# Kernel optimization log

Measured on AMD Instinct MI355X. Metric: run time of the kernel, lower is better.

Reference implementation:

```python
import jax, jax.numpy as jnp
import numpy as np

N_NODES = 20000


def _segment_softmax(alpha, dst, num_nodes):
    # numerically-stable softmax over edges grouped by destination node
    m = jax.ops.segment_max(alpha, dst, num_segments=num_nodes)
    m = jnp.where(jnp.isfinite(m), m, 0.0)
    a = jnp.exp(alpha - m[dst])
    denom = jax.ops.segment_sum(a, dst, num_segments=num_nodes)
    return a / denom[dst]


def mgcn_conv(x, src, dst, edge_type, basis, att, weight, root, bias, num_nodes):
    # x: [N, in], basis: [B, in, out], att: [R, B], weight: [R, out=in]
    x_i = x[dst]                                   # [E, in] target feats
    x_j = x[src]                                   # [E, in] source feats
    # per-edge attention logit: sum_d x_i[d] * w_r[d] * x_j[d]
    alpha = jnp.sum(x_i * weight[edge_type] * x_j, axis=1)   # [E]
    alpha = _segment_softmax(alpha, dst, num_nodes)          # [E]
    # basis-decomposed per-edge transform: x_j @ (att_r . basis)
    t = jnp.einsum('ei,bio->ebo', x_j, basis)                # [E, B, out]
    msg = jnp.einsum('ebo,eb->eo', t, att[edge_type])        # [E, out]
    msg = msg * alpha[:, None]
    out = jax.ops.segment_sum(msg, dst, num_segments=num_nodes)  # [N, out]
    return out + x @ root + bias


def setup_inputs() -> dict:
    key = jax.random.key(0)
    ks = jax.random.split(key, 16)
    E, D, R, B, N = 32768, 128, 474, 64, N_NODES
    s = 0.05
    return {
        'entity': jnp.arange(N, dtype=jnp.int64) if jax.config.jax_enable_x64 else jnp.arange(N, dtype=jnp.int32),
        'edge_index': jax.random.randint(ks[0], (2, E), 0, N, dtype=jnp.int32),
        'edge_type': jax.random.randint(ks[1], (E,), 0, R, dtype=jnp.int32),
        'emb_table': jax.random.normal(ks[2], (N, D), dtype=jnp.float32),
        'basis1': jax.random.normal(ks[3], (B, D, D), dtype=jnp.float32) * s,
        'att1': jax.random.normal(ks[4], (R, B), dtype=jnp.float32) * s,
        'weight1': jax.random.normal(ks[5], (R, D), dtype=jnp.float32) * s,
        'root1': jax.random.normal(ks[6], (D, D), dtype=jnp.float32) * s,
        'bias1': jnp.zeros((D,), dtype=jnp.float32),
        'basis2': jax.random.normal(ks[7], (B, D, D), dtype=jnp.float32) * s,
        'att2': jax.random.normal(ks[8], (R, B), dtype=jnp.float32) * s,
        'weight2': jax.random.normal(ks[9], (R, D), dtype=jnp.float32) * s,
        'root2': jax.random.normal(ks[10], (D, D), dtype=jnp.float32) * s,
        'bias2': jnp.zeros((D,), dtype=jnp.float32),
    }


def reference(entity, edge_index, edge_type, emb_table,
              basis1, att1, weight1, root1, bias1,
              basis2, att2, weight2, root2, bias2):
    src, dst = edge_index[0], edge_index[1]   # PyG: (source j, target i)
    x = emb_table[entity]                     # embedding lookup
    h = jax.nn.relu(mgcn_conv(x, src, dst, edge_type, basis1, att1,
                              weight1, root1, bias1, N_NODES))
    # dropout is identity at inference
    out = mgcn_conv(h, src, dst, edge_type, basis2, att2,
                    weight2, root2, bias2, N_NODES)
    return out
```

## Files before the change

### kernel.cpp

```cpp
#include <hip/hip_runtime.h>
#include <hip/hip_bf16.h>

#define N_NODES 20000
#define N_EDGES 32768
#define DIM 128
#define N_REL 474
#define N_BASIS 64
#define TILE_E 64
#define CHCAP 128
#define MAXCH (N_EDGES / CHCAP + N_REL)
#define WSTRIDE 264
#define HIST_BLKS 16
#define EDGES_PER_HIST (N_EDGES / HIST_BLKS)

#define WMIX_BLKS 1024
#define ROOTT_BLKS 2
#define GATHER_BASE (WMIX_BLKS + ROOTT_BLKS)
#define PREP_GRID 1664

#define RG_BLKS ((N_NODES + 63) / 64)
#define MSG_GRID (MAXCH + RG_BLKS)
#define MERGE_GRID 1024

typedef __bf16 bf16x8 __attribute__((ext_vector_type(8)));
typedef float f32x4 __attribute__((ext_vector_type(4)));

__device__ __forceinline__ unsigned short f2b(float f) {
    unsigned u = __float_as_uint(f);
    unsigned r = (u + 0x7FFFu + ((u >> 16) & 1u)) >> 16;
    return (unsigned short)r;
}
__device__ __forceinline__ float b2f(unsigned short s) {
    return __uint_as_float(((unsigned)s) << 16);
}
__device__ __forceinline__ __bf16 u2b(unsigned short u) {
    union { unsigned short u; __bf16 b; } c; c.u = u; return c.b;
}
__device__ __forceinline__ float dot2bf(unsigned a, unsigned b, float wx, float wy) {
    return b2f((unsigned short)(a & 0xFFFFu)) * wx * b2f((unsigned short)(b & 0xFFFFu))
         + b2f((unsigned short)(a >> 16)) * wy * b2f((unsigned short)(b >> 16));
}

__global__ __launch_bounds__(256) void prep_kernel(const float4* __restrict__ emb,
                                                   const int* __restrict__ entity,
                                                   const int* __restrict__ etype,
                                                   ushort4* __restrict__ xb4,
                                                   float4* __restrict__ zreg, int zcount4,
                                                   int* __restrict__ partial,
                                                   const float* __restrict__ att1,
                                                   const float* __restrict__ basis1,
                                                   unsigned short* __restrict__ W1,
                                                   const float* __restrict__ att2,
                                                   const float* __restrict__ basis2,
                                                   unsigned short* __restrict__ W2,
                                                   const float* __restrict__ root1,
                                                   unsigned short* __restrict__ rootT1,
                                                   const float* __restrict__ root2,
                                                   unsigned short* __restrict__ rootT2) {
    __shared__ __align__(16) unsigned short bt[64 * WSTRIDE];
    int t = threadIdx.x;
    if (blockIdx.x < WMIX_BLKS) {
        int wi = blockIdx.x;
        int layer = wi >> 9;
        int cb = (wi >> 3) & 63;
        int rg = wi & 7;
        const float* att   = layer ? att2 : att1;
        const float* basis = layer ? basis2 : basis1;
        unsigned short* W  = layer ? W2 : W1;
        int io0 = cb * 256;
        int r0 = rg * 64;
#pragma unroll
        for (int p = 0; p < 16; p++) {
            int c = t + 256 * p;
            int k = c >> 6, of = c & 63;
            float4 v = *(const float4*)(basis + (size_t)k * (DIM * DIM) + io0 + of * 4);
            ushort4 s;
            s.x = f2b(v.x); s.y = f2b(v.y); s.z = f2b(v.z); s.w = f2b(v.w);
            int ofx = of ^ (((k >> 3) & 7) << 2);
            *(ushort4*)&bt[k * WSTRIDE + ofx * 4] = s;
        }
        __syncthreads();

        int w = t >> 6, l = t & 63, n = l & 15, q = l >> 4;
        bf16x8 bfr[2][4];
#pragma unroll
        for (int kb = 0; kb < 2; kb++) {
            int kbase = kb * 32 + q * 8;
            int sx = ((kb * 4 + q) & 7) << 4;
#pragma unroll
            for (int c = 0; c < 4; c++) {
                int ob = (w * 64 + c * 16 + n) ^ sx;
#pragma unroll
                for (int j = 0; j < 8; j++) bfr[kb][c][j] = u2b(bt[(kbase + j) * WSTRIDE + ob]);
            }
        }
        __syncthreads();

        f32x4 acc[4][4] = {};
#pragma unroll
        for (int kb = 0; kb < 2; kb++) {
            int kbase = kb * 32 + q * 8;
            bf16x8 a[4];
#pragma unroll
            for (int rt = 0; rt < 4; rt++) {
                int rm = min(r0 + rt * 16 + n, N_REL - 1);
                const float4* ap = (const float4*)(att + (size_t)rm * N_BASIS + kbase);
                float4 u0 = ap[0], u1 = ap[1];
                a[rt][0] = (__bf16)u0.x; a[rt][1] = (__bf16)u0.y;
                a[rt][2] = (__bf16)u0.z; a[rt][3] = (__bf16)u0.w;
                a[rt][4] = (__bf16)u1.x; a[rt][5] = (__bf16)u1.y;
                a[rt][6] = (__bf16)u1.z; a[rt][7] = (__bf16)u1.w;
            }
#pragma unroll
            for (int c = 0; c < 4; c++) {
#pragma unroll
                for (int rt = 0; rt < 4; rt++)
                    acc[rt][c] = __builtin_amdgcn_mfma_f32_16x16x32_bf16(a[rt], bfr[kb][c], acc[rt][c], 0, 0, 0);
            }
        }
#pragma unroll
        for (int rt = 0; rt < 4; rt++) {
#pragma unroll
            for (int c = 0; c < 4; c++) {
#pragma unroll
                for (int g = 0; g < 4; g++)
                    bt[(rt * 16 + q * 4 + g) * WSTRIDE + w * 64 + c * 16 + n] = f2b(acc[rt][c][g]);
            }
        }
        __syncthreads();
        int srow = t >> 2, sseg = t & 3;
        int rr = r0 + srow;
        if (rr < N_REL) {
            const int4* sp = (const int4*)&bt[srow * WSTRIDE];
            unsigned short* wp = W + (size_t)rr * (DIM * DIM) + io0;
#pragma unroll
            for (int ii = 0; ii < 8; ii++) {
                int i = (ii + sseg * 2) & 7;
                int4 v = sp[sseg * 8 + i];
                *(int4*)(wp + sseg * 64 + i * 8) = v;
            }
        }
    } else if (blockIdx.x < GATHER_BASE) {
        int wi2 = blockIdx.x - WMIX_BLKS;
        const float* rm = wi2 ? root2 : root1;
        unsigned short* rt_ = wi2 ? rootT2 : rootT1;
        unsigned short* sb16 = bt;
#pragma unroll
        for (int p = 0; p < 16; p++) {
            int idx = t + 256 * p;
            int k = idx >> 5, o4 = idx & 31;
            float4 v = ((const float4*)rm)[idx];
            ushort4 s;
            s.x = f2b(v.x); s.y = f2b(v.y); s.z = f2b(v.z); s.w = f2b(v.w);
            *(ushort4*)&sb16[k * 132 + o4 * 4] = s;
        }
        __syncthreads();
        int o = t >> 1, kh = (t & 1) * 64;
#pragma unroll
        for (int i = 0; i < 16; i++) {
            int k0 = kh + i * 4;
            ushort4 s;
            s.x = sb16[(k0 + 0) * 132 + o];
            s.y = sb16[(k0 + 1) * 132 + o];
            s.z = sb16[(k0 + 2) * 132 + o];
            s.w = sb16[(k0 + 3) * 132 + o];
            *(ushort4*)&rt_[o * DIM + k0] = s;
        }
    } else {
        int pb = blockIdx.x - GATHER_BASE;
        int gtid = pb * 256 + t;
        int gsz = (PREP_GRID - GATHER_BASE) * 256;
        int total4 = N_NODES * DIM / 4;
        for (int i = gtid; i < total4; i += gsz) {
            int n = i >> 5, rem = i & 31;
            float4 v = emb[(size_t)entity[n] * 32 + rem];
            ushort4 s;
            s.x = f2b(v.x); s.y = f2b(v.y); s.z = f2b(v.z); s.w = f2b(v.w);
            xb4[i] = s;
        }
        float4 z = make_float4(0.f, 0.f, 0.f, 0.f);
        for (int i = gtid; i < zcount4; i += gsz) zreg[i] = z;
        if (pb < HIST_BLKS) {
            int* ih = (int*)bt;
            for (int i = t; i < N_REL; i += 256) ih[i] = 0;
            __syncthreads();
            int e0 = pb * EDGES_PER_HIST;
            for (int e = e0 + t; e < e0 + EDGES_PER_HIST; e += 256)
                atomicAdd(&ih[etype[e]], 1);
            __syncthreads();
            for (int i = t; i < N_REL; i += 256) partial[pb * N_REL + i] = ih[i];
        }
    }
}

__global__ void scanr_kernel(const int* __restrict__ partial, int* __restrict__ offs,
                             int* __restrict__ cursor, int* __restrict__ chunk_r,
                             int* __restrict__ chunk_o, int* __restrict__ nchunks) {
    __shared__ int s[512];
    __shared__ int lnc;
    int t = threadIdx.x;
    int v = 0;
    if (t < N_REL) {
#pragma unroll
        for (int k = 0; k < HIST_BLKS; k++) v += partial[k * N_REL + t];
    }
    s[t] = v;
    if (t == 0) lnc = 0;
    __syncthreads();
    for (int d = 1; d < 512; d <<= 1) {
        int add = (t >= d) ? s[t - d] : 0;
        __syncthreads();
        s[t] += add;
        __syncthreads();
    }
    int excl = s[t] - v;
    if (t < N_REL) { offs[t] = excl; cursor[t] = excl; }
    if (t == 0) offs[N_REL] = N_EDGES;
    if (t < N_REL && v > 0) {
        int nc = (v + CHCAP - 1) / CHCAP;
        int cb = atomicAdd(&lnc, nc);
        for (int c = 0; c < nc; c++) { chunk_r[cb + c] = t; chunk_o[cb + c] = excl + c * CHCAP; }
    }
    __syncthreads();
    if (t == 0) *nchunks = lnc;
}

__global__ __launch_bounds__(256) void scatter_kernel(const int* __restrict__ etype,
                                                      int* __restrict__ cursor,
                                                      int* __restrict__ eids) {
    for (int e = blockIdx.x * 256 + threadIdx.x; e < N_EDGES; e += (int)gridDim.x * 256) {
        int r = etype[e];
        int p = atomicAdd(&cursor[r], 1);
        eids[p] = e;
    }
}

__global__ __launch_bounds__(256) void msg_kernel(const unsigned short* __restrict__ xb,
                                                  const unsigned short* __restrict__ W,
                                                  const float* __restrict__ wlog,
                                                  const int* __restrict__ src,
                                                  const int* __restrict__ dst,
                                                  const int* __restrict__ eids,
                                                  const int* __restrict__ offs,
                                                  const int* __restrict__ chunk_r,
                                                  const int* __restrict__ chunk_o,
                                                  const int* __restrict__ nchunks,
                                                  float* __restrict__ den,
                                                  float* __restrict__ accm,
                                                  const unsigned short* __restrict__ rootT,
                                                  float* __restrict__ racc) {
    __shared__ __align__(16) unsigned short wt[128 * 136];
    __shared__ __align__(16) float wf[DIM];
    __shared__ float scf[TILE_E];
    __shared__ int sdd[TILE_E];
    __shared__ int ssrc[TILE_E];

    int t = threadIdx.x;
    if ((int)blockIdx.x < MAXCH) {
        if ((int)blockIdx.x >= *nchunks) return;
        int r = chunk_r[blockIdx.x];
        int base = chunk_o[blockIdx.x];
        int cnt = min(base + CHCAP, offs[r + 1]) - base;
        const unsigned short* Wr = W + (size_t)r * (DIM * DIM);
#pragma unroll
        for (int p = 0; p < 8; p++) {
            int c = t + 256 * p;
            int k = c >> 4, oct = c & 15;
            int4 v = *(const int4*)(Wr + k * DIM + oct * 8);
            int oct2 = oct ^ (((k >> 3) & 7) << 1);
            *(int4*)&wt[k * 136 + oct2 * 8] = v;
        }
        if (t < 32) ((float4*)wf)[t] = ((const float4*)(wlog + (size_t)r * DIM))[t];
        __syncthreads();

        int w = t >> 6, l = t & 63, n = l & 15, q = l >> 4;
        int el4 = t >> 2, l4 = t & 3;

        for (int t0 = 0; t0 < cnt; t0 += TILE_E) {
            int nE = min(TILE_E, cnt - t0);
            if (t < TILE_E) {
                if (t < nE) {
                    int e = eids[base + t0 + t];
                    ssrc[t] = src[e];
                    sdd[t]  = dst[e];
                } else { ssrc[t] = 0; sdd[t] = 0; }
            }
            __syncthreads();

            {
                int s_ = ssrc[el4], d_ = sdd[el4];
                const int4* xj = (const int4*)(xb + (size_t)s_ * DIM) + l4 * 4;
                const int4* xi = (const int4*)(xb + (size_t)d_ * DIM) + l4 * 4;
                const float4* wv = (const float4*)&wf[l4 * 32];
                float v = 0.f;
#pragma unroll
                for (int u = 0; u < 4; u++) {
                    int4 a = xj[u]; int4 bb = xi[u];
                    float4 w0 = wv[u * 2], w1 = wv[u * 2 + 1];
                    v += dot2bf((unsigned)a.x, (unsigned)bb.x, w0.x, w0.y)
                       + dot2bf((unsigned)a.y, (unsigned)bb.y, w0.z, w0.w)
                       + dot2bf((unsigned)a.z, (unsigned)bb.z, w1.x, w1.y)
                       + dot2bf((unsigned)a.w, (unsigned)bb.w, w1.z, w1.w);
                }
                v += __shfl_xor(v, 1, 64);
                v += __shfl_xor(v, 2, 64);
                if (l4 == 0) {
                    if (el4 < nE) {
                        float a = expf(v);
                        scf[el4] = a;
                        atomicAdd(&den[d_], a);
                    } else scf[el4] = 0.f;
                }
            }
            __syncthreads();

            f32x4 acc[2][4] = {};
#pragma unroll
            for (int kb = 0; kb < 4; kb++) {
                bf16x8 a[4];
#pragma unroll
                for (int rt = 0; rt < 4; rt++)
                    a[rt] = *(const bf16x8*)(xb + (size_t)ssrc[rt * 16 + n] * DIM + kb * 32 + q * 8);
                int kbase = kb * 32 + q * 8;
                int sx = ((kb * 4 + q) & 7) << 4;
#pragma unroll
                for (int c = 0; c < 2; c++) {
                    int ob = ((w * 2 + c) * 16 + n) ^ sx;
                    bf16x8 bb;
#pragma unroll
                    for (int j = 0; j < 8; j++) bb[j] = u2b(wt[(kbase + j) * 136 + ob]);
#pragma unroll
                    for (int rt = 0; rt < 4; rt++)
                        acc[c][rt] = __builtin_amdgcn_mfma_f32_16x16x32_bf16(a[rt], bb, acc[c][rt], 0, 0, 0);
                }
            }
#pragma unroll
            for (int c = 0; c < 2; c++) {
                int col = (w * 2 + c) * 16 + n;
#pragma unroll
                for (int rt = 0; rt < 4; rt++) {
#pragma unroll
                    for (int rg = 0; rg < 4; rg++) {
                        int e = rt * 16 + q * 4 + rg;
                        if (e < nE)
                            atomicAdd(&accm[(size_t)sdd[e] * DIM + col], scf[e] * acc[c][rt][rg]);
                    }
                }
            }
            __syncthreads();
        }
    } else {
        int n0 = ((int)blockIdx.x - MAXCH) * 64;
        unsigned short* xrf = wt;
#pragma unroll
        for (int p = 0; p < 4; p++) {
            int c = t + 256 * p;
            int g = c >> 6;
            int rt = g >> 2, kb = g & 3;
            int q2 = (c >> 4) & 3, m = c & 15;
            int row = n0 + rt * 16 + m;
            int oct = kb * 4 + q2;
            int4 v = make_int4(0, 0, 0, 0);
            if (row < N_NODES) v = *(const int4*)(xb + (size_t)row * DIM + oct * 8);
            *(int4*)&xrf[c * 8] = v;
        }
        __syncthreads();

        int w_ = t >> 6, l = t & 63, n = l & 15, q = l >> 4;
        f32x4 acc[2][4] = {};
#pragma unroll
        for (int kb = 0; kb < 4; kb++) {
            bf16x8 a[4];
#pragma unroll
            for (int rt = 0; rt < 4; rt++) a[rt] = *(const bf16x8*)&xrf[((rt * 4 + kb) * 64 + l) * 8];
            int kbase = kb * 32 + q * 8;
#pragma unroll
            for (int c = 0; c < 2; c++) {
                int col = (w_ * 2 + c) * 16 + n;
                bf16x8 bb = *(const bf16x8*)(rootT + (size_t)col * DIM + kbase);
#pragma unroll
                for (int rt = 0; rt < 4; rt++)
                    acc[c][rt] = __builtin_amdgcn_mfma_f32_16x16x32_bf16(a[rt], bb, acc[c][rt], 0, 0, 0);
            }
        }
#pragma unroll
        for (int c = 0; c < 2; c++) {
            int col = (w_ * 2 + c) * 16 + n;
#pragma unroll
            for (int rt = 0; rt < 4; rt++) {
#pragma unroll
                for (int rg = 0; rg < 4; rg++) {
                    int row = n0 + rt * 16 + q * 4 + rg;
                    if (row < N_NODES)
                        racc[(size_t)row * DIM + col] = acc[c][rt][rg];
                }
            }
        }
    }
}

__global__ __launch_bounds__(256) void merge_kernel(const float4* __restrict__ racc,
                                                    const float4* __restrict__ accm,
                                                    const float* __restrict__ den,
                                                    const float* __restrict__ bias,
                                                    float4* __restrict__ outf,
                                                    ushort4* __restrict__ outb) {
    int gtid = blockIdx.x * 256 + threadIdx.x;
    const int tot4 = N_NODES * (DIM / 4);
    for (int i = gtid; i < tot4; i += (int)gridDim.x * 256) {
        int row = i >> 5;
        int c0 = (i & 31) * 4;
        float4 rv = racc[i];
        float4 mv = accm[i];
        float4 bo = *(const float4*)&bias[c0];
        float dv = den[row];
        float inv = dv > 0.f ? 1.0f / dv : 0.f;
        float4 v;
        v.x = rv.x + bo.x + mv.x * inv;
        v.y = rv.y + bo.y + mv.y * inv;
        v.z = rv.z + bo.z + mv.z * inv;
        v.w = rv.w + bo.w + mv.w * inv;
        if (outb) {
            ushort4 s;
            s.x = f2b(fmaxf(v.x, 0.f)); s.y = f2b(fmaxf(v.y, 0.f));
            s.z = f2b(fmaxf(v.z, 0.f)); s.w = f2b(fmaxf(v.w, 0.f));
            outb[i] = s;
        } else {
            outf[i] = v;
        }
    }
}

extern "C" void kernel_launch(void* const* d_in, const int* in_sizes, int n_in,
                              void* d_out, int out_size, void* d_ws, size_t ws_size,
                              hipStream_t stream) {
    const int N = N_NODES, E = N_EDGES, R = N_REL;

    const int* entity = (const int*)d_in[0];
    const int* eidx   = (const int*)d_in[1];
    const int* src    = eidx;
    const int* dst    = eidx + E;
    const int* etype  = (const int*)d_in[2];
    const float* emb  = (const float*)d_in[3];
    const float* basis1 = (const float*)d_in[4];
    const float* att1   = (const float*)d_in[5];
    const float* w1     = (const float*)d_in[6];
    const float* root1  = (const float*)d_in[7];
    const float* bias1  = (const float*)d_in[8];
    const float* basis2 = (const float*)d_in[9];
    const float* att2   = (const float*)d_in[10];
    const float* w2     = (const float*)d_in[11];
    const float* root2  = (const float*)d_in[12];
    const float* bias2  = (const float*)d_in[13];
    float* out = (float*)d_out;

    size_t off = 0;
    auto alloc = [&](size_t bytes) -> void* {
        void* p = (char*)d_ws + off;
        off += (bytes + 255) & ~(size_t)255;
        return p;
    };
    unsigned short* W1 = (unsigned short*)alloc((size_t)R * DIM * DIM * 2);
    unsigned short* W2 = (unsigned short*)alloc((size_t)R * DIM * DIM * 2);
    unsigned short* xb = (unsigned short*)alloc((size_t)N * DIM * 2);
    unsigned short* hb = (unsigned short*)alloc((size_t)N * DIM * 2);
    float* racc1  = (float*)alloc((size_t)N * DIM * 4);
    float* racc2  = (float*)alloc((size_t)N * DIM * 4);
    float* zreg   = (float*)alloc(((size_t)2 * N + (size_t)2 * N * DIM) * 4);
    float* den1   = zreg;
    float* den2   = zreg + N;
    float* accm1  = zreg + 2 * N;
    float* accm2  = zreg + 2 * N + (size_t)N * DIM;
    unsigned short* rootT1 = (unsigned short*)alloc((size_t)DIM * DIM * 2);
    unsigned short* rootT2 = (unsigned short*)alloc((size_t)DIM * DIM * 2);
    int* partial  = (int*)alloc((size_t)HIST_BLKS * R * 4);
    int* offs     = (int*)alloc((size_t)(R + 1) * 4);
    int* cursor   = (int*)alloc((size_t)R * 4);
    int* eids     = (int*)alloc((size_t)E * 4);
    int* chunk_r  = (int*)alloc((size_t)MAXCH * 4);
    int* chunk_o  = (int*)alloc((size_t)MAXCH * 4);
    int* nchunks  = (int*)alloc(256);

    int zcount4 = (2 * N + 2 * N * DIM) / 4;

    prep_kernel<<<PREP_GRID, 256, 0, stream>>>(
        (const float4*)emb, entity, etype, (ushort4*)xb, (float4*)zreg, zcount4, partial,
        att1, basis1, W1, att2, basis2, W2, root1, rootT1, root2, rootT2);

    scanr_kernel<<<1, 512, 0, stream>>>(partial, offs, cursor, chunk_r, chunk_o, nchunks);
    scatter_kernel<<<64, 256, 0, stream>>>(etype, cursor, eids);

    msg_kernel<<<MSG_GRID, 256, 0, stream>>>(xb, W1, w1, src, dst, eids, offs,
                                             chunk_r, chunk_o, nchunks,
                                             den1, accm1, rootT1, racc1);
    merge_kernel<<<MERGE_GRID, 256, 0, stream>>>((const float4*)racc1, (const float4*)accm1,
                                                 den1, bias1, nullptr, (ushort4*)hb);

    msg_kernel<<<MSG_GRID, 256, 0, stream>>>(hb, W2, w2, src, dst, eids, offs,
                                             chunk_r, chunk_o, nchunks,
                                             den2, accm2, rootT2, racc2);
    merge_kernel<<<MERGE_GRID, 256, 0, stream>>>((const float4*)racc2, (const float4*)accm2,
                                                 den2, bias2, (float4*)out, nullptr);
}
```

Measured before the change: 212.0 us.

## Split prep into basis conversion and fused wmix/plan/root-GEMM kernel

```diff
diff --git a/kernel.cpp b/kernel.cpp
--- a/kernel.cpp
+++ b/kernel.cpp
@@ -9,17 +9,16 @@
 #define TILE_E 64
 #define CHCAP 128
 #define MAXCH (N_EDGES / CHCAP + N_REL)
-#define WSTRIDE 264
 #define HIST_BLKS 16
 #define EDGES_PER_HIST (N_EDGES / HIST_BLKS)
 
-#define WMIX_BLKS 1024
-#define ROOTT_BLKS 2
-#define GATHER_BASE (WMIX_BLKS + ROOTT_BLKS)
-#define PREP_GRID 1664
-
+#define PRE_GRID 1024
+#define BST 136
+#define WMIX2_BLKS 2048
 #define RG_BLKS ((N_NODES + 63) / 64)
-#define MSG_GRID (MAXCH + RG_BLKS)
+#define WP_GRID (WMIX2_BLKS + 1 + RG_BLKS)
+#define MSG1_GRID MAXCH
+#define MSG2_GRID (MAXCH + RG_BLKS)
 #define MERGE_GRID 1024
 
 typedef __bf16 bf16x8 __attribute__((ext_vector_type(8)));
@@ -41,62 +40,140 @@
          + b2f((unsigned short)(a >> 16)) * wy * b2f((unsigned short)(b >> 16));
 }
 
-__global__ __launch_bounds__(256) void prep_kernel(const float4* __restrict__ emb,
-                                                   const int* __restrict__ entity,
-                                                   const int* __restrict__ etype,
-                                                   ushort4* __restrict__ xb4,
-                                                   float4* __restrict__ zreg, int zcount4,
-                                                   int* __restrict__ partial,
-                                                   const float* __restrict__ att1,
-                                                   const float* __restrict__ basis1,
-                                                   unsigned short* __restrict__ W1,
-                                                   const float* __restrict__ att2,
-                                                   const float* __restrict__ basis2,
-                                                   unsigned short* __restrict__ W2,
-                                                   const float* __restrict__ root1,
-                                                   unsigned short* __restrict__ rootT1,
-                                                   const float* __restrict__ root2,
-                                                   unsigned short* __restrict__ rootT2) {
-    __shared__ __align__(16) unsigned short bt[64 * WSTRIDE];
+__global__ __launch_bounds__(256) void pre_kernel(const float4* __restrict__ emb,
+                                                  const int* __restrict__ entity,
+                                                  const int* __restrict__ etype,
+                                                  ushort4* __restrict__ xb4,
+                                                  float4* __restrict__ zreg, int zcount4,
+                                                  int* __restrict__ partial,
+                                                  const float* __restrict__ basis1,
+                                                  ushort4* __restrict__ bas16_1,
+                                                  const float* __restrict__ basis2,
+                                                  ushort4* __restrict__ bas16_2,
+                                                  const float* __restrict__ root1,
+                                                  unsigned short* __restrict__ rootT1,
+                                                  const float* __restrict__ root2,
+                                                  unsigned short* __restrict__ rootT2) {
+    __shared__ __align__(16) unsigned short sb16[128 * 132];
     int t = threadIdx.x;
-    if (blockIdx.x < WMIX_BLKS) {
-        int wi = blockIdx.x;
-        int layer = wi >> 9;
-        int cb = (wi >> 3) & 63;
-        int rg = wi & 7;
-        const float* att   = layer ? att2 : att1;
-        const float* basis = layer ? basis2 : basis1;
-        unsigned short* W  = layer ? W2 : W1;
-        int io0 = cb * 256;
-        int r0 = rg * 64;
+    if (blockIdx.x < 2) {
+        const float* rm = blockIdx.x ? root2 : root1;
+        unsigned short* rt_ = blockIdx.x ? rootT2 : rootT1;
 #pragma unroll
         for (int p = 0; p < 16; p++) {
-            int c = t + 256 * p;
-            int k = c >> 6, of = c & 63;
-            float4 v = *(const float4*)(basis + (size_t)k * (DIM * DIM) + io0 + of * 4);
+            int idx = t + 256 * p;
+            int k = idx >> 5, o4 = idx & 31;
+            float4 v = ((const float4*)rm)[idx];
             ushort4 s;
             s.x = f2b(v.x); s.y = f2b(v.y); s.z = f2b(v.z); s.w = f2b(v.w);
+            *(ushort4*)&sb16[k * 132 + o4 * 4] = s;
+        }
+        __syncthreads();
+        int o = t >> 1, kh = (t & 1) * 64;
+#pragma unroll
+        for (int i = 0; i < 16; i++) {
+            int k0 = kh + i * 4;
+            ushort4 s;
+            s.x = sb16[(k0 + 0) * 132 + o];
+            s.y = sb16[(k0 + 1) * 132 + o];
+            s.z = sb16[(k0 + 2) * 132 + o];
+            s.w = sb16[(k0 + 3) * 132 + o];
+            *(ushort4*)&rt_[o * DIM + k0] = s;
+        }
+    } else {
+        int pb = blockIdx.x - 2;
+        int gtid = pb * 256 + t;
+        int gsz = (PRE_GRID - 2) * 256;
+        int total4 = N_NODES * DIM / 4;
+        for (int i = gtid; i < total4; i += gsz) {
+            int n = i >> 5, rem = i & 31;
+            float4 v = emb[(size_t)entity[n] * 32 + rem];
+            ushort4 s;
+            s.x = f2b(v.x); s.y = f2b(v.y); s.z = f2b(v.z); s.w = f2b(v.w);
+            xb4[i] = s;
+        }
+        float4 z = make_float4(0.f, 0.f, 0.f, 0.f);
+        for (int i = gtid; i < zcount4; i += gsz) zreg[i] = z;
+        int totb4 = N_BASIS * DIM * DIM / 4;
+        for (int i = gtid; i < totb4; i += gsz) {
+            float4 v = ((const float4*)basis1)[i];
+            ushort4 s;
+            s.x = f2b(v.x); s.y = f2b(v.y); s.z = f2b(v.z); s.w = f2b(v.w);
+            bas16_1[i] = s;
+        }
+        for (int i = gtid; i < totb4; i += gsz) {
+            float4 v = ((const float4*)basis2)[i];
+            ushort4 s;
+            s.x = f2b(v.x); s.y = f2b(v.y); s.z = f2b(v.z); s.w = f2b(v.w);
+            bas16_2[i] = s;
+        }
+        if (pb < HIST_BLKS) {
+            int* ih = (int*)sb16;
+            for (int i = t; i < N_REL; i += 256) ih[i] = 0;
+            __syncthreads();
+            int e0 = pb * EDGES_PER_HIST;
+            for (int e = e0 + t; e < e0 + EDGES_PER_HIST; e += 256)
+                atomicAdd(&ih[etype[e]], 1);
+            __syncthreads();
+            for (int i = t; i < N_REL; i += 256) partial[pb * N_REL + i] = ih[i];
+        }
+    }
+}
+
+__global__ __launch_bounds__(256) void wmixplan_kernel(const unsigned short* __restrict__ bas16_1,
+                                                       const float* __restrict__ att1,
+                                                       unsigned short* __restrict__ W1,
+                                                       const unsigned short* __restrict__ bas16_2,
+                                                       const float* __restrict__ att2,
+                                                       unsigned short* __restrict__ W2,
+                                                       const int* __restrict__ partial,
+                                                       int* __restrict__ offs,
+                                                       int* __restrict__ chunk_r,
+                                                       int* __restrict__ chunk_o,
+                                                       int* __restrict__ nchunks,
+                                                       int* __restrict__ eids,
+                                                       const int* __restrict__ etype,
+                                                       const unsigned short* __restrict__ xb,
+                                                       const unsigned short* __restrict__ rootT1,
+                                                       float* __restrict__ racc1) {
+    __shared__ __align__(16) unsigned short bt[64 * BST];
+    int t = threadIdx.x;
+    if (blockIdx.x < WMIX2_BLKS) {
+        int wi = blockIdx.x;
+        int layer = wi >> 10;
+        int cb = (wi >> 3) & 127;
+        int rg = wi & 7;
+        const unsigned short* bas = layer ? bas16_2 : bas16_1;
+        const float* att   = layer ? att2 : att1;
+        unsigned short* W  = layer ? W2 : W1;
+        int io0 = cb * 128;
+        int r0 = rg * 64;
+#pragma unroll
+        for (int p = 0; p < 8; p++) {
+            int c = t + 256 * p;
+            int k = c >> 5, of = c & 31;
+            ushort4 s = *(const ushort4*)(bas + (size_t)k * (DIM * DIM) + io0 + of * 4);
             int ofx = of ^ (((k >> 3) & 7) << 2);
-            *(ushort4*)&bt[k * WSTRIDE + ofx * 4] = s;
+            *(ushort4*)&bt[k * BST + ofx * 4] = s;
         }
         __syncthreads();
 
         int w = t >> 6, l = t & 63, n = l & 15, q = l >> 4;
-        bf16x8 bfr[2][4];
+        bf16x8 bfr[2][2];
 #pragma unroll
         for (int kb = 0; kb < 2; kb++) {
             int kbase = kb * 32 + q * 8;
             int sx = ((kb * 4 + q) & 7) << 4;
 #pragma unroll
-            for (int c = 0; c < 4; c++) {
-                int ob = (w * 64 + c * 16 + n) ^ sx;
-#pragma unroll
-                for (int j = 0; j < 8; j++) bfr[kb][c][j] = u2b(bt[(kbase + j) * WSTRIDE + ob]);
-            }
-        }
-        __syncthreads();
-
-        f32x4 acc[4][4] = {};
+            for (int c = 0; c < 2; c++) {
+                int ob = (w * 32 + c * 16 + n) ^ sx;
+#pragma unroll
+                for (int j = 0; j < 8; j++) bfr[kb][c][j] = u2b(bt[(kbase + j) * BST + ob]);
+            }
+        }
+        __syncthreads();
+
+        f32x4 acc[4][2] = {};
 #pragma unroll
         for (int kb = 0; kb < 2; kb++) {
             int kbase = kb * 32 + q * 8;
@@ -112,7 +189,7 @@
                 a[rt][6] = (__bf16)u1.z; a[rt][7] = (__bf16)u1.w;
             }
 #pragma unroll
-            for (int c = 0; c < 4; c++) {
+            for (int c = 0; c < 2; c++) {
 #pragma unroll
                 for (int rt = 0; rt < 4; rt++)
                     acc[rt][c] = __builtin_amdgcn_mfma_f32_16x16x32_bf16(a[rt], bfr[kb][c], acc[rt][c], 0, 0, 0);
@@ -121,117 +198,118 @@
 #pragma unroll
         for (int rt = 0; rt < 4; rt++) {
 #pragma unroll
-            for (int c = 0; c < 4; c++) {
+            for (int c = 0; c < 2; c++) {
 #pragma unroll
                 for (int g = 0; g < 4; g++)
-                    bt[(rt * 16 + q * 4 + g) * WSTRIDE + w * 64 + c * 16 + n] = f2b(acc[rt][c][g]);
+                    bt[(rt * 16 + q * 4 + g) * BST + w * 32 + c * 16 + n] = f2b(acc[rt][c][g]);
             }
         }
         __syncthreads();
         int srow = t >> 2, sseg = t & 3;
         int rr = r0 + srow;
         if (rr < N_REL) {
-            const int4* sp = (const int4*)&bt[srow * WSTRIDE];
             unsigned short* wp = W + (size_t)rr * (DIM * DIM) + io0;
-#pragma unroll
-            for (int ii = 0; ii < 8; ii++) {
-                int i = (ii + sseg * 2) & 7;
-                int4 v = sp[sseg * 8 + i];
-                *(int4*)(wp + sseg * 64 + i * 8) = v;
-            }
-        }
-    } else if (blockIdx.x < GATHER_BASE) {
-        int wi2 = blockIdx.x - WMIX_BLKS;
-        const float* rm = wi2 ? root2 : root1;
-        unsigned short* rt_ = wi2 ? rootT2 : rootT1;
-        unsigned short* sb16 = bt;
-#pragma unroll
-        for (int p = 0; p < 16; p++) {
-            int idx = t + 256 * p;
-            int k = idx >> 5, o4 = idx & 31;
-            float4 v = ((const float4*)rm)[idx];
-            ushort4 s;
-            s.x = f2b(v.x); s.y = f2b(v.y); s.z = f2b(v.z); s.w = f2b(v.w);
-            *(ushort4*)&sb16[k * 132 + o4 * 4] = s;
-        }
-        __syncthreads();
-        int o = t >> 1, kh = (t & 1) * 64;
-#pragma unroll
-        for (int i = 0; i < 16; i++) {
-            int k0 = kh + i * 4;
-            ushort4 s;
-            s.x = sb16[(k0 + 0) * 132 + o];
-            s.y = sb16[(k0 + 1) * 132 + o];
-            s.z = sb16[(k0 + 2) * 132 + o];
-            s.w = sb16[(k0 + 3) * 132 + o];
-            *(ushort4*)&rt_[o * DIM + k0] = s;
+            const int4* sp = (const int4*)&bt[srow * BST];
+#pragma unroll
+            for (int ii = 0; ii < 4; ii++) {
+                int i = (ii + sseg) & 3;
+                *(int4*)(wp + sseg * 32 + i * 8) = sp[sseg * 4 + i];
+            }
+        }
+    } else if (blockIdx.x == WMIX2_BLKS) {
+        int* sA   = (int*)bt;
+        int* sB   = sA + 512;
+        int* lcur = sB + 512;
+        __shared__ int lnc;
+        int t2 = t + 256;
+        int v0 = 0, v1 = 0;
+        if (t < N_REL) {
+#pragma unroll
+            for (int k = 0; k < HIST_BLKS; k++) v0 += partial[k * N_REL + t];
+        }
+        if (t2 < N_REL) {
+#pragma unroll
+            for (int k = 0; k < HIST_BLKS; k++) v1 += partial[k * N_REL + t2];
+        }
+        sA[t] = v0; sA[t2] = v1;
+        if (t == 0) lnc = 0;
+        __syncthreads();
+        int* src_ = sA; int* dst_ = sB;
+        for (int d = 1; d < 512; d <<= 1) {
+            int a0 = src_[t]  + ((t  >= d) ? src_[t  - d] : 0);
+            int a1 = src_[t2] + ((t2 >= d) ? src_[t2 - d] : 0);
+            dst_[t] = a0; dst_[t2] = a1;
+            __syncthreads();
+            int* tmp = src_; src_ = dst_; dst_ = tmp;
+        }
+        int e0 = src_[t] - v0, e1 = src_[t2] - v1;
+        if (t < N_REL)  { offs[t] = e0;  lcur[t] = e0; }
+        if (t2 < N_REL) { offs[t2] = e1; lcur[t2] = e1; }
+        if (t == 0) offs[N_REL] = N_EDGES;
+        if (t < N_REL && v0 > 0) {
+            int nc = (v0 + CHCAP - 1) / CHCAP;
+            int cb = atomicAdd(&lnc, nc);
+            for (int c = 0; c < nc; c++) { chunk_r[cb + c] = t;  chunk_o[cb + c] = e0 + c * CHCAP; }
+        }
+        if (t2 < N_REL && v1 > 0) {
+            int nc = (v1 + CHCAP - 1) / CHCAP;
+            int cb = atomicAdd(&lnc, nc);
+            for (int c = 0; c < nc; c++) { chunk_r[cb + c] = t2; chunk_o[cb + c] = e1 + c * CHCAP; }
+        }
+        __syncthreads();
+        if (t == 0) *nchunks = lnc;
+        for (int e = t; e < N_EDGES; e += 256) {
+            int r = etype[e];
+            int p = atomicAdd(&lcur[r], 1);
+            eids[p] = e;
         }
     } else {
-        int pb = blockIdx.x - GATHER_BASE;
-        int gtid = pb * 256 + t;
-        int gsz = (PREP_GRID - GATHER_BASE) * 256;
-        int total4 = N_NODES * DIM / 4;
-        for (int i = gtid; i < total4; i += gsz) {
-            int n = i >> 5, rem = i & 31;
-            float4 v = emb[(size_t)entity[n] * 32 + rem];
-            ushort4 s;
-            s.x = f2b(v.x); s.y = f2b(v.y); s.z = f2b(v.z); s.w = f2b(v.w);
-            xb4[i] = s;
-        }
-        float4 z = make_float4(0.f, 0.f, 0.f, 0.f);
-        for (int i = gtid; i < zcount4; i += gsz) zreg[i] = z;
-        if (pb < HIST_BLKS) {
-            int* ih = (int*)bt;
-            for (int i = t; i < N_REL; i += 256) ih[i] = 0;
-            __syncthreads();
-            int e0 = pb * EDGES_PER_HIST;
-            for (int e = e0 + t; e < e0 + EDGES_PER_HIST; e += 256)
-                atomicAdd(&ih[etype[e]], 1);
-            __syncthreads();
-            for (int i = t; i < N_REL; i += 256) partial[pb * N_REL + i] = ih[i];
-        }
-    }
-}
-
-__global__ void scanr_kernel(const int* __restrict__ partial, int* __restrict__ offs,
-                             int* __restrict__ cursor, int* __restrict__ chunk_r,
-                             int* __restrict__ chunk_o, int* __restrict__ nchunks) {
-    __shared__ int s[512];
-    __shared__ int lnc;
-    int t = threadIdx.x;
-    int v = 0;
-    if (t < N_REL) {
-#pragma unroll
-        for (int k = 0; k < HIST_BLKS; k++) v += partial[k * N_REL + t];
-    }
-    s[t] = v;
-    if (t == 0) lnc = 0;
-    __syncthreads();
-    for (int d = 1; d < 512; d <<= 1) {
-        int add = (t >= d) ? s[t - d] : 0;
-        __syncthreads();
-        s[t] += add;
-        __syncthreads();
-    }
-    int excl = s[t] - v;
-    if (t < N_REL) { offs[t] = excl; cursor[t] = excl; }
-    if (t == 0) offs[N_REL] = N_EDGES;
-    if (t < N_REL && v > 0) {
-        int nc = (v + CHCAP - 1) / CHCAP;
-        int cb = atomicAdd(&lnc, nc);
-        for (int c = 0; c < nc; c++) { chunk_r[cb + c] = t; chunk_o[cb + c] = excl + c * CHCAP; }
-    }
-    __syncthreads();
-    if (t == 0) *nchunks = lnc;
-}
-
-__global__ __launch_bounds__(256) void scatter_kernel(const int* __restrict__ etype,
-                                                      int* __restrict__ cursor,
-                                                      int* __restrict__ eids) {
-    for (int e = blockIdx.x * 256 + threadIdx.x; e < N_EDGES; e += (int)gridDim.x * 256) {
-        int r = etype[e];
-        int p = atomicAdd(&cursor[r], 1);
-        eids[p] = e;
+        int n0 = ((int)blockIdx.x - WMIX2_BLKS - 1) * 64;
+        unsigned short* xrf = bt;
+#pragma unroll
+        for (int p = 0; p < 4; p++) {
+            int c = t + 256 * p;
+            int g = c >> 6;
+            int rt = g >> 2, kb = g & 3;
+            int q2 = (c >> 4) & 3, m = c & 15;
+            int row = n0 + rt * 16 + m;
+            int oct = kb * 4 + q2;
+            int4 v = make_int4(0, 0, 0, 0);
+            if (row < N_NODES) v = *(const int4*)(xb + (size_t)row * DIM + oct * 8);
+            *(int4*)&xrf[c * 8] = v;
+        }
+        __syncthreads();
+
+        int w_ = t >> 6, l = t & 63, n = l & 15, q = l >> 4;
+        f32x4 acc[2][4] = {};
+#pragma unroll
+        for (int kb = 0; kb < 4; kb++) {
+            bf16x8 a[4];
+#pragma unroll
+            for (int rt = 0; rt < 4; rt++) a[rt] = *(const bf16x8*)&xrf[((rt * 4 + kb) * 64 + l) * 8];
+            int kbase = kb * 32 + q * 8;
+#pragma unroll
+            for (int c = 0; c < 2; c++) {
+                int col = (w_ * 2 + c) * 16 + n;
+                bf16x8 bb = *(const bf16x8*)(rootT1 + (size_t)col * DIM + kbase);
+#pragma unroll
+                for (int rt = 0; rt < 4; rt++)
+                    acc[c][rt] = __builtin_amdgcn_mfma_f32_16x16x32_bf16(a[rt], bb, acc[c][rt], 0, 0, 0);
+            }
+        }
+#pragma unroll
+        for (int c = 0; c < 2; c++) {
+            int col = (w_ * 2 + c) * 16 + n;
+#pragma unroll
+            for (int rt = 0; rt < 4; rt++) {
+#pragma unroll
+                for (int rg = 0; rg < 4; rg++) {
+                    int row = n0 + rt * 16 + q * 4 + rg;
+                    if (row < N_NODES)
+                        racc1[(size_t)row * DIM + col] = acc[c][rt][rg];
+                }
+            }
+        }
     }
 }
 
@@ -473,9 +551,10 @@
     float* accm2  = zreg + 2 * N + (size_t)N * DIM;
     unsigned short* rootT1 = (unsigned short*)alloc((size_t)DIM * DIM * 2);
     unsigned short* rootT2 = (unsigned short*)alloc((size_t)DIM * DIM * 2);
+    unsigned short* bas16_1 = (unsigned short*)alloc((size_t)N_BASIS * DIM * DIM * 2);
+    unsigned short* bas16_2 = (unsigned short*)alloc((size_t)N_BASIS * DIM * DIM * 2);
     int* partial  = (int*)alloc((size_t)HIST_BLKS * R * 4);
     int* offs     = (int*)alloc((size_t)(R + 1) * 4);
-    int* cursor   = (int*)alloc((size_t)R * 4);
     int* eids     = (int*)alloc((size_t)E * 4);
     int* chunk_r  = (int*)alloc((size_t)MAXCH * 4);
     int* chunk_o  = (int*)alloc((size_t)MAXCH * 4);
@@ -483,22 +562,25 @@
 
     int zcount4 = (2 * N + 2 * N * DIM) / 4;
 
-    prep_kernel<<<PREP_GRID, 256, 0, stream>>>(
+    pre_kernel<<<PRE_GRID, 256, 0, stream>>>(
         (const float4*)emb, entity, etype, (ushort4*)xb, (float4*)zreg, zcount4, partial,
-        att1, basis1, W1, att2, basis2, W2, root1, rootT1, root2, rootT2);
-
-    scanr_kernel<<<1, 512, 0, stream>>>(partial, offs, cursor, chunk_r, chunk_o, nchunks);
-    scatter_kernel<<<64, 256, 0, stream>>>(etype, cursor, eids);
-
-    msg_kernel<<<MSG_GRID, 256, 0, stream>>>(xb, W1, w1, src, dst, eids, offs,
-                                             chunk_r, chunk_o, nchunks,
-                                             den1, accm1, rootT1, racc1);
+        basis1, (ushort4*)bas16_1, basis2, (ushort4*)bas16_2,
+        root1, rootT1, root2, rootT2);
+
+    wmixplan_kernel<<<WP_GRID, 256, 0, stream>>>(
+        bas16_1, att1, W1, bas16_2, att2, W2,
+        partial, offs, chunk_r, chunk_o, nchunks, eids, etype,
+        xb, rootT1, racc1);
+
+    msg_kernel<<<MSG1_GRID, 256, 0, stream>>>(xb, W1, w1, src, dst, eids, offs,
+                                              chunk_r, chunk_o, nchunks,
+                                              den1, accm1, rootT1, racc1);
     merge_kernel<<<MERGE_GRID, 256, 0, stream>>>((const float4*)racc1, (const float4*)accm1,
                                                  den1, bias1, nullptr, (ushort4*)hb);
 
-    msg_kernel<<<MSG_GRID, 256, 0, stream>>>(hb, W2, w2, src, dst, eids, offs,
-                                             chunk_r, chunk_o, nchunks,
-                                             den2, accm2, rootT2, racc2);
+    msg_kernel<<<MSG2_GRID, 256, 0, stream>>>(hb, W2, w2, src, dst, eids, offs,
+                                              chunk_r, chunk_o, nchunks,
+                                              den2, accm2, rootT2, racc2);
     merge_kernel<<<MERGE_GRID, 256, 0, stream>>>((const float4*)racc2, (const float4*)accm2,
                                                  den2, bias2, (float4*)out, nullptr);
 }
```

Measured after the change: 240.3 us. 1.13x slower.

## Replace atomic scatter-add aggregation with CSR-by-destination gather of bf16 messages

Applied to the files above, without the earlier changes.

```diff
diff --git a/kernel.cpp b/kernel.cpp
--- a/kernel.cpp
+++ b/kernel.cpp
@@ -19,8 +19,8 @@
 #define PREP_GRID 1664
 
 #define RG_BLKS ((N_NODES + 63) / 64)
-#define MSG_GRID (MAXCH + RG_BLKS)
-#define MERGE_GRID 1024
+#define MSGE_GRID (MAXCH + RG_BLKS)
+#define GATH_BLKS ((N_NODES + 63) / 64)
 
 typedef __bf16 bf16x8 __attribute__((ext_vector_type(8)));
 typedef float f32x4 __attribute__((ext_vector_type(4)));
@@ -44,9 +44,10 @@
 __global__ __launch_bounds__(256) void prep_kernel(const float4* __restrict__ emb,
                                                    const int* __restrict__ entity,
                                                    const int* __restrict__ etype,
+                                                   const int* __restrict__ dst,
                                                    ushort4* __restrict__ xb4,
-                                                   float4* __restrict__ zreg, int zcount4,
                                                    int* __restrict__ partial,
+                                                   int* __restrict__ dhist,
                                                    const float* __restrict__ att1,
                                                    const float* __restrict__ basis1,
                                                    unsigned short* __restrict__ W1,
@@ -178,24 +179,27 @@
             s.x = f2b(v.x); s.y = f2b(v.y); s.z = f2b(v.z); s.w = f2b(v.w);
             xb4[i] = s;
         }
-        float4 z = make_float4(0.f, 0.f, 0.f, 0.f);
-        for (int i = gtid; i < zcount4; i += gsz) zreg[i] = z;
         if (pb < HIST_BLKS) {
             int* ih = (int*)bt;
             for (int i = t; i < N_REL; i += 256) ih[i] = 0;
             __syncthreads();
             int e0 = pb * EDGES_PER_HIST;
-            for (int e = e0 + t; e < e0 + EDGES_PER_HIST; e += 256)
+            for (int e = e0 + t; e < e0 + EDGES_PER_HIST; e += 256) {
                 atomicAdd(&ih[etype[e]], 1);
+                atomicAdd(&dhist[dst[e]], 1);
+            }
             __syncthreads();
             for (int i = t; i < N_REL; i += 256) partial[pb * N_REL + i] = ih[i];
         }
     }
 }
 
-__global__ void scanr_kernel(const int* __restrict__ partial, int* __restrict__ offs,
-                             int* __restrict__ cursor, int* __restrict__ chunk_r,
-                             int* __restrict__ chunk_o, int* __restrict__ nchunks) {
+__global__ void plan_kernel(const int* __restrict__ partial,
+                            const int* __restrict__ dhist,
+                            int* __restrict__ offs, int* __restrict__ cursor,
+                            int* __restrict__ chunk_r, int* __restrict__ chunk_o,
+                            int* __restrict__ nchunks,
+                            int* __restrict__ doffs, int* __restrict__ dcur) {
     __shared__ int s[512];
     __shared__ int lnc;
     int t = threadIdx.x;
@@ -223,37 +227,69 @@
     }
     __syncthreads();
     if (t == 0) *nchunks = lnc;
+    __syncthreads();
+    const int NB = 40;
+    int b0 = t * NB;
+    int mycnt = 0;
+    for (int i = 0; i < NB; i++) {
+        int bi = b0 + i;
+        if (bi < N_NODES) mycnt += dhist[bi];
+    }
+    s[t] = mycnt;
+    __syncthreads();
+    for (int d = 1; d < 512; d <<= 1) {
+        int add = (t >= d) ? s[t - d] : 0;
+        __syncthreads();
+        s[t] += add;
+        __syncthreads();
+    }
+    int run = s[t] - mycnt;
+    for (int i = 0; i < NB; i++) {
+        int bi = b0 + i;
+        if (bi < N_NODES) {
+            doffs[bi] = run;
+            dcur[bi] = run;
+            run += dhist[bi];
+        }
+    }
+    if (t == 0) doffs[N_NODES] = N_EDGES;
 }
 
 __global__ __launch_bounds__(256) void scatter_kernel(const int* __restrict__ etype,
+                                                      const int* __restrict__ dst,
                                                       int* __restrict__ cursor,
-                                                      int* __restrict__ eids) {
+                                                      int* __restrict__ eids,
+                                                      int* __restrict__ dcur,
+                                                      int* __restrict__ eids2) {
     for (int e = blockIdx.x * 256 + threadIdx.x; e < N_EDGES; e += (int)gridDim.x * 256) {
         int r = etype[e];
         int p = atomicAdd(&cursor[r], 1);
         eids[p] = e;
-    }
-}
-
-__global__ __launch_bounds__(256) void msg_kernel(const unsigned short* __restrict__ xb,
-                                                  const unsigned short* __restrict__ W,
-                                                  const float* __restrict__ wlog,
-                                                  const int* __restrict__ src,
-                                                  const int* __restrict__ dst,
-                                                  const int* __restrict__ eids,
-                                                  const int* __restrict__ offs,
-                                                  const int* __restrict__ chunk_r,
-                                                  const int* __restrict__ chunk_o,
-                                                  const int* __restrict__ nchunks,
-                                                  float* __restrict__ den,
-                                                  float* __restrict__ accm,
-                                                  const unsigned short* __restrict__ rootT,
-                                                  float* __restrict__ racc) {
+        int d_ = dst[e];
+        int p2 = atomicAdd(&dcur[d_], 1);
+        eids2[p2] = e;
+    }
+}
+
+__global__ __launch_bounds__(256) void msgE_kernel(const unsigned short* __restrict__ xb,
+                                                   const unsigned short* __restrict__ W,
+                                                   const float* __restrict__ wlog,
+                                                   const int* __restrict__ src,
+                                                   const int* __restrict__ dst,
+                                                   const int* __restrict__ eids,
+                                                   const int* __restrict__ offs,
+                                                   const int* __restrict__ chunk_r,
+                                                   const int* __restrict__ chunk_o,
+                                                   const int* __restrict__ nchunks,
+                                                   float* __restrict__ alpha,
+                                                   unsigned short* __restrict__ msgbuf,
+                                                   const unsigned short* __restrict__ rootT,
+                                                   float* __restrict__ racc) {
     __shared__ __align__(16) unsigned short wt[128 * 136];
     __shared__ __align__(16) float wf[DIM];
-    __shared__ float scf[TILE_E];
     __shared__ int sdd[TILE_E];
     __shared__ int ssrc[TILE_E];
+    __shared__ int seid[TILE_E];
 
     int t = threadIdx.x;
     if ((int)blockIdx.x < MAXCH) {
@@ -281,9 +317,10 @@
             if (t < TILE_E) {
                 if (t < nE) {
                     int e = eids[base + t0 + t];
+                    seid[t] = e;
                     ssrc[t] = src[e];
                     sdd[t]  = dst[e];
-                } else { ssrc[t] = 0; sdd[t] = 0; }
+                } else { seid[t] = 0; ssrc[t] = 0; sdd[t] = 0; }
             }
             __syncthreads();
 
@@ -304,15 +341,8 @@
                 }
                 v += __shfl_xor(v, 1, 64);
                 v += __shfl_xor(v, 2, 64);
-                if (l4 == 0) {
-                    if (el4 < nE) {
-                        float a = expf(v);
-                        scf[el4] = a;
-                        atomicAdd(&den[d_], a);
-                    } else scf[el4] = 0.f;
-                }
-            }
-            __syncthreads();
+                if (l4 == 0 && el4 < nE) alpha[seid[el4]] = expf(v);
+            }
 
             f32x4 acc[2][4] = {};
 #pragma unroll
@@ -343,7 +373,7 @@
                     for (int rg = 0; rg < 4; rg++) {
                         int e = rt * 16 + q * 4 + rg;
                         if (e < nE)
-                            atomicAdd(&accm[(size_t)sdd[e] * DIM + col], scf[e] * acc[c][rt][rg]);
+                            msgbuf[(size_t)seid[e] * DIM + col] = f2b(acc[c][rt][rg]);
                     }
                 }
             }
@@ -399,34 +429,58 @@
     }
 }
 
-__global__ __launch_bounds__(256) void merge_kernel(const float4* __restrict__ racc,
-                                                    const float4* __restrict__ accm,
-                                                    const float* __restrict__ den,
-                                                    const float* __restrict__ bias,
-                                                    float4* __restrict__ outf,
-                                                    ushort4* __restrict__ outb) {
-    int gtid = blockIdx.x * 256 + threadIdx.x;
-    const int tot4 = N_NODES * (DIM / 4);
-    for (int i = gtid; i < tot4; i += (int)gridDim.x * 256) {
-        int row = i >> 5;
-        int c0 = (i & 31) * 4;
-        float4 rv = racc[i];
-        float4 mv = accm[i];
-        float4 bo = *(const float4*)&bias[c0];
-        float dv = den[row];
-        float inv = dv > 0.f ? 1.0f / dv : 0.f;
-        float4 v;
-        v.x = rv.x + bo.x + mv.x * inv;
-        v.y = rv.y + bo.y + mv.y * inv;
-        v.z = rv.z + bo.z + mv.z * inv;
-        v.w = rv.w + bo.w + mv.w * inv;
+__global__ __launch_bounds__(256) void gather_kernel(const float* __restrict__ racc,
+                                                     const float* __restrict__ bias,
+                                                     const float* __restrict__ alpha,
+                                                     const unsigned short* __restrict__ msgbuf,
+                                                     const int* __restrict__ doffs,
+                                                     const int* __restrict__ eids2,
+                                                     float* __restrict__ outf,
+                                                     unsigned short* __restrict__ outb) {
+    int t = threadIdx.x;
+    int d = blockIdx.x * 64 + (t >> 2);
+    if (d >= N_NODES) return;
+    int cs = (t & 3) * 32;
+
+    float4 ms[8] = {};
+    float asum = 0.f;
+    int e0 = doffs[d], e1 = doffs[d + 1];
+    for (int ee = e0; ee < e1; ee++) {
+        int eid = eids2[ee];
+        float al = alpha[eid];
+        asum += al;
+        const int4* mp = (const int4*)(msgbuf + (size_t)eid * DIM + cs);
+#pragma unroll
+        for (int j = 0; j < 4; j++) {
+            int4 v = mp[j];
+            ms[2 * j].x     += al * b2f((unsigned short)((unsigned)v.x & 0xFFFFu));
+            ms[2 * j].y     += al * b2f((unsigned short)((unsigned)v.x >> 16));
+            ms[2 * j].z     += al * b2f((unsigned short)((unsigned)v.y & 0xFFFFu));
+            ms[2 * j].w     += al * b2f((unsigned short)((unsigned)v.y >> 16));
+            ms[2 * j + 1].x += al * b2f((unsigned short)((unsigned)v.z & 0xFFFFu));
+            ms[2 * j + 1].y += al * b2f((unsigned short)((unsigned)v.z >> 16));
+            ms[2 * j + 1].z += al * b2f((unsigned short)((unsigned)v.w & 0xFFFFu));
+            ms[2 * j + 1].w += al * b2f((unsigned short)((unsigned)v.w >> 16));
+        }
+    }
+    float inv = asum > 0.f ? 1.0f / asum : 0.f;
+    const float4* rp = (const float4*)(racc + (size_t)d * DIM + cs);
+    const float4* bp = (const float4*)(bias + cs);
+#pragma unroll
+    for (int i = 0; i < 8; i++) {
+        float4 r = rp[i], b = bp[i];
+        float4 val;
+        val.x = r.x + b.x + ms[i].x * inv;
+        val.y = r.y + b.y + ms[i].y * inv;
+        val.z = r.z + b.z + ms[i].z * inv;
+        val.w = r.w + b.w + ms[i].w * inv;
         if (outb) {
             ushort4 s;
-            s.x = f2b(fmaxf(v.x, 0.f)); s.y = f2b(fmaxf(v.y, 0.f));
-            s.z = f2b(fmaxf(v.z, 0.f)); s.w = f2b(fmaxf(v.w, 0.f));
-            outb[i] = s;
+            s.x = f2b(fmaxf(val.x, 0.f)); s.y = f2b(fmaxf(val.y, 0.f));
+            s.z = f2b(fmaxf(val.z, 0.f)); s.w = f2b(fmaxf(val.w, 0.f));
+            *(ushort4*)(outb + (size_t)d * DIM + cs + i * 4) = s;
         } else {
-            outf[i] = v;
+            *(float4*)(outf + (size_t)d * DIM + cs + i * 4) = val;
         }
     }
 }
@@ -466,39 +520,42 @@
     unsigned short* hb = (unsigned short*)alloc((size_t)N * DIM * 2);
     float* racc1  = (float*)alloc((size_t)N * DIM * 4);
     float* racc2  = (float*)alloc((size_t)N * DIM * 4);
-    float* zreg   = (float*)alloc(((size_t)2 * N + (size_t)2 * N * DIM) * 4);
-    float* den1   = zreg;
-    float* den2   = zreg + N;
-    float* accm1  = zreg + 2 * N;
-    float* accm2  = zreg + 2 * N + (size_t)N * DIM;
     unsigned short* rootT1 = (unsigned short*)alloc((size_t)DIM * DIM * 2);
     unsigned short* rootT2 = (unsigned short*)alloc((size_t)DIM * DIM * 2);
+    unsigned short* msgbuf = (unsigned short*)alloc((size_t)E * DIM * 2);
+    float* alpha  = (float*)alloc((size_t)E * 4);
     int* partial  = (int*)alloc((size_t)HIST_BLKS * R * 4);
+    int* dhist    = (int*)alloc((size_t)N * 4);
+    int* doffs    = (int*)alloc((size_t)(N + 1) * 4);
+    int* dcur     = (int*)alloc((size_t)N * 4);
     int* offs     = (int*)alloc((size_t)(R + 1) * 4);
     int* cursor   = (int*)alloc((size_t)R * 4);
     int* eids     = (int*)alloc((size_t)E * 4);
+    int* eids2    = (int*)alloc((size_t)E * 4);
     int* chunk_r  = (int*)alloc((size_t)MAXCH * 4);
     int* chunk_o  = (int*)alloc((size_t)MAXCH * 4);
     int* nchunks  = (int*)alloc(256);
 
-    int zcount4 = (2 * N + 2 * N * DIM) / 4;
+    hipMemsetAsync(dhist, 0, (size_t)N * 4, stream);
 
     prep_kernel<<<PREP_GRID, 256, 0, stream>>>(
-        (const float4*)emb, entity, etype, (ushort4*)xb, (float4*)zreg, zcount4, partial,
+        (const float4*)emb, entity, etype, dst, (ushort4*)xb, partial, dhist,
         att1, basis1, W1, att2, basis2, W2, root1, rootT1, root2, rootT2);
 
-    scanr_kernel<<<1, 512, 0, stream>>>(partial, offs, cursor, chunk_r, chunk_o, nchunks);
-    scatter_kernel<<<64, 256, 0, stream>>>(etype, cursor, eids);
-
-    msg_kernel<<<MSG_GRID, 256, 0, stream>>>(xb, W1, w1, src, dst, eids, offs,
-                                             chunk_r, chunk_o, nchunks,
-                                             den1, accm1, rootT1, racc1);
-    merge_kernel<<<MERGE_GRID, 256, 0, stream>>>((const float4*)racc1, (const float4*)accm1,
-                                                 den1, bias1, nullptr, (ushort4*)hb);
-
-    msg_kernel<<<MSG_GRID, 256, 0, stream>>>(hb, W2, w2, src, dst, eids, offs,
-                                             chunk_r, chunk_o, nchunks,
-                                             den2, accm2, rootT2, racc2);
-    merge_kernel<<<MERGE_GRID, 256, 0, stream>>>((const float4*)racc2, (const float4*)accm2,
-                                                 den2, bias2, (float4*)out, nullptr);
-}
+    plan_kernel<<<1, 512, 0, stream>>>(partial, dhist, offs, cursor,
+                                       chunk_r, chunk_o, nchunks, doffs, dcur);
+
+    scatter_kernel<<<64, 256, 0, stream>>>(etype, dst, cursor, eids, dcur, eids2);
+
+    msgE_kernel<<<MSGE_GRID, 256, 0, stream>>>(xb, W1, w1, src, dst, eids, offs,
+                                               chunk_r, chunk_o, nchunks,
+                                               alpha, msgbuf, rootT1, racc1);
+    gather_kernel<<<GATH_BLKS, 256, 0, stream>>>(racc1, bias1, alpha, msgbuf,
+                                                 doffs, eids2, nullptr, hb);
+
+    msgE_kernel<<<MSGE_GRID, 256, 0, stream>>>(hb, W2, w2, src, dst, eids, offs,
+                                               chunk_r, chunk_o, nchunks,
+                                               alpha, msgbuf, rootT2, racc2);
+    gather_kernel<<<GATH_BLKS, 256, 0, stream>>>(racc2, bias2, alpha, msgbuf,
+                                                 doffs, eids2, out, nullptr);
+}
```

After: 262.1 us. +23.7%, slower.
